# Kernel tuning notes

Measured on AMD Instinct MI355X. Metric: run time of the kernel, lower is better.

The kernel has to match this reference:

```python
import jax, jax.numpy as jnp
import numpy as np

NUM_USERS = 100000
NUM_BOOKS = 50000
HIDDEN = 128
USER_FEAT = 256
BOOK_FEAT = 256
E_PER_REL = 500000
NUM_LAYERS = 2


def setup_inputs() -> dict:
    key = jax.random.key(0)
    ks = jax.random.split(key, 10)
    user_x = jax.random.normal(ks[0], (NUM_USERS, USER_FEAT), dtype=jnp.float32)
    book_x = jax.random.normal(ks[1], (NUM_BOOKS, BOOK_FEAT), dtype=jnp.float32)
    user_W = jax.random.normal(ks[2], (HIDDEN, USER_FEAT), dtype=jnp.float32) * 0.05
    user_b = jax.random.normal(ks[3], (HIDDEN,), dtype=jnp.float32) * 0.05
    book_W = jax.random.normal(ks[4], (HIDDEN, BOOK_FEAT), dtype=jnp.float32) * 0.05
    book_b = jax.random.normal(ks[5], (HIDDEN,), dtype=jnp.float32) * 0.05
    # edge_index[0] = user indices, edge_index[1] = book indices
    rates_edge = jnp.stack([
        jax.random.randint(ks[6], (E_PER_REL,), 0, NUM_USERS),
        jax.random.randint(ks[7], (E_PER_REL,), 0, NUM_BOOKS)])
    implicit_edge = jnp.stack([
        jax.random.randint(ks[8], (E_PER_REL,), 0, NUM_USERS),
        jax.random.randint(ks[9], (E_PER_REL,), 0, NUM_BOOKS)])
    return {"user_x": user_x, "book_x": book_x, "user_W": user_W,
            "user_b": user_b, "book_W": book_W, "book_b": book_b,
            "rates_edge": rates_edge, "implicit_edge": implicit_edge}


def _lightgcn(user_x, book_x, user_W, user_b, book_W, book_b, rates_edge, implicit_edge):
    num_users = user_x.shape[0]
    num_nodes = num_users + book_x.shape[0]
    # input projections
    cu = user_x @ user_W.T + user_b  # [U, H]
    cb = book_x @ book_W.T + book_b  # [B, H]
    user_embeds = [cu]
    book_embeds = [cb]
    # build full directed edge list exactly as in the torch source
    all_edges = jnp.concatenate([rates_edge, implicit_edge], axis=1)  # [2, E]
    book_to_user = jnp.stack([all_edges[1] + num_users, all_edges[0]])
    full_edge = jnp.concatenate([all_edges, book_to_user], axis=1)  # [2, 2E]
    row, col = full_edge[0], full_edge[1]
    # symmetric degree normalization (edges fixed across layers)
    deg = jax.ops.segment_sum(jnp.ones(col.shape, dtype=cu.dtype), col,
                              num_segments=num_nodes)
    deg_inv_sqrt = jnp.where(deg > 0, jax.lax.rsqrt(jnp.maximum(deg, 1.0) * 0 + jnp.where(deg > 0, deg, 1.0)), 0.0)
    deg_inv_sqrt = jnp.where(deg > 0, jax.lax.rsqrt(jnp.where(deg > 0, deg, 1.0)), 0.0)
    norm = deg_inv_sqrt[row] * deg_inv_sqrt[col]  # [2E]
    for _ in range(NUM_LAYERS):
        x = jnp.concatenate([cu, cb], axis=0)  # [U+B, H]
        msg = x[row] * norm[:, None]           # gather + scale, [2E, H]
        out = jax.ops.segment_sum(msg, col, num_segments=num_nodes)  # scatter-add
        cu = out[:num_users]
        cb = out[num_users:]
        user_embeds.append(cu)
        book_embeds.append(cb)
    final_user = jnp.mean(jnp.stack(user_embeds), axis=0)
    final_book = jnp.mean(jnp.stack(book_embeds), axis=0)
    return final_user, final_book


def reference(user_x, book_x, user_W, user_b, book_W, book_b, rates_edge, implicit_edge):
    return _lightgcn(user_x, book_x, user_W, user_b, book_W, book_b,
                     rates_edge, implicit_edge)
```

## Files before the change

kernel.cpp:

```cpp
#include <hip/hip_runtime.h>

#define NUSERS 100000
#define NBOOKS 50000
#define HID 128
#define FEAT 256
#define EPR 500000
#define NEDGE (2 * EPR)

#define UBLK64 ((NUSERS + 63) / 64)
#define BBLK64 ((NBOOKS + 63) / 64)
#define GH_BLOCKS (UBLK64 + BBLK64)
#define FILL_B ((NEDGE + 255) / 256)
#define NXCD 8

typedef __attribute__((ext_vector_type(8))) short bf16x8;
typedef __attribute__((ext_vector_type(4))) float f32x4;

__device__ __forceinline__ unsigned short f2bf(float f) {
  union { float f; unsigned u; } v; v.f = f;
  unsigned r = v.u + 0x7FFFu + ((v.u >> 16) & 1u);
  return (unsigned short)(r >> 16);
}
__device__ __forceinline__ float bf2f(unsigned short h) {
  union { unsigned u; float f; } v; v.u = ((unsigned)h) << 16;
  return v.f;
}
__device__ __forceinline__ unsigned pk2bf(float lo, float hi) {
  unsigned r;
  asm("v_cvt_pk_bf16_f32 %0, %1, %2" : "=v"(r) : "v"(lo), "v"(hi));
  return r;
}
__device__ __forceinline__ int xcc_id() {
  unsigned id;
  asm volatile("s_getreg_b32 %0, hwreg(HW_REG_XCC_ID)" : "=s"(id));
  return (int)(id & 7);
}

__global__ void cast_w(const float* __restrict__ w0, const float* __restrict__ w1,
                       unsigned short* __restrict__ o0, unsigned short* __restrict__ o1)
{
  int i = blockIdx.x * 256 + threadIdx.x;
  if (i < HID * FEAT) { o0[i] = f2bf(w0[i]); o1[i] = f2bf(w1[i]); }
}

__device__ __forceinline__ void decode_edge(const int* __restrict__ rates,
                                            const int* __restrict__ impl,
                                            int i, int& u, int& bk)
{
  if (i < EPR) { u = rates[i]; bk = rates[EPR + i]; }
  else { int j = i - EPR; u = impl[j]; bk = impl[EPR + j]; }
}

__global__ __launch_bounds__(256) void gemm_hist(
    const float* __restrict__ Xu, const float* __restrict__ Xb,
    const unsigned short* __restrict__ Wu, const unsigned short* __restrict__ Wb,
    const float* __restrict__ bu, const float* __restrict__ bb,
    unsigned short* __restrict__ cu0b, float* __restrict__ outb,
    float* __restrict__ outu,
    const int* __restrict__ rates, const int* __restrict__ impl,
    int* __restrict__ degu8, int* __restrict__ cntb8,
    unsigned* __restrict__ relpos)
{
  __shared__ float Asb[4][2048];
  const int bid = blockIdx.x;
  const int tid = threadIdx.x;
  const int lane = tid & 63;
  const int wv   = tid >> 6;
  const int l15  = lane & 15, l4 = lane >> 4;

  {
    const unsigned x = (unsigned)xcc_id();
    int* cnt = cntb8 + (size_t)x * NBOOKS;
    int* deg = degu8 + (size_t)x * NUSERS;
    const int e0 = bid * 512 + tid;
#pragma unroll
    for (int q = 0; q < 2; ++q) {
      int e = e0 + q * 256;
      if (e < NEDGE) {
        int u, bk;
        decode_edge(rates, impl, e, u, bk);
        unsigned p = (unsigned)__hip_atomic_fetch_add(&cnt[bk], 1, __ATOMIC_RELAXED,
                                                      __HIP_MEMORY_SCOPE_WORKGROUP);
        __hip_atomic_fetch_add(&deg[u], 1, __ATOMIC_RELAXED,
                               __HIP_MEMORY_SCOPE_WORKGROUP);
        relpos[e] = (x << 29) | (p & 0x1FFFFFFFu);
      }
    }
  }

  const bool isU = bid < UBLK64;
  const float* __restrict__ X = isU ? Xu : Xb;
  const unsigned short* __restrict__ W = isU ? Wu : Wb;
  const float* __restrict__ bias = isU ? bu : bb;
  const int M    = isU ? NUSERS : NBOOKS;
  const int bm   = (isU ? bid : bid - UBLK64) * 64;
  const int wrow = bm + wv * 16;

  float* wbase = &Asb[wv][0];

  f32x4 acc[8];
#pragma unroll
  for (int ni = 0; ni < 8; ++ni) acc[ni] = (f32x4)0.f;

#pragma unroll
  for (int h = 0; h < 2; ++h) {
    if (h) {
      asm volatile("s_waitcnt lgkmcnt(0)" ::: "memory");
      __builtin_amdgcn_sched_barrier(0);
    }
#pragma unroll
    for (int rnd = 0; rnd < 8; ++rnd) {
      int o = rnd * 64 + lane;
      int r = o >> 5;
      int c = o & 31;
      int lc = c ^ r;
      int gr = wrow + r; if (gr > M - 1) gr = M - 1;
      __builtin_amdgcn_global_load_lds(
          (const float*)&X[(size_t)gr * FEAT + h * 128 + lc * 4],
          wbase + rnd * 256, 16, 0, 0);
    }
    asm volatile("s_waitcnt vmcnt(0)" ::: "memory");
    __builtin_amdgcn_sched_barrier(0);

#pragma unroll
    for (int ks = 0; ks < 4; ++ks) {
      const int kg = h * 4 + ks;
      bf16x8 bfr[8];
#pragma unroll
      for (int ni = 0; ni < 8; ++ni)
        bfr[ni] = *reinterpret_cast<const bf16x8*>(
            &W[(size_t)(ni * 16 + l15) * FEAT + kg * 32 + l4 * 8]);

      int u0 = (ks * 8 + l4 * 2) ^ l15;
      int u1 = (ks * 8 + l4 * 2 + 1) ^ l15;
      f32x4 a0 = *reinterpret_cast<const f32x4*>(&wbase[(l15 * 32 + u0) * 4]);
      f32x4 a1 = *reinterpret_cast<const f32x4*>(&wbase[(l15 * 32 + u1) * 4]);
      union { unsigned u32[4]; bf16x8 v; } au;
      au.u32[0] = pk2bf(a0[0], a0[1]);
      au.u32[1] = pk2bf(a0[2], a0[3]);
      au.u32[2] = pk2bf(a1[0], a1[1]);
      au.u32[3] = pk2bf(a1[2], a1[3]);

#pragma unroll
      for (int ni = 0; ni < 8; ++ni)
        acc[ni] = __builtin_amdgcn_mfma_f32_16x16x32_bf16(au.v, bfr[ni], acc[ni], 0, 0, 0);
    }
  }

#pragma unroll
  for (int ni = 0; ni < 8; ++ni) {
    int col = ni * 16 + l15;
    float bj = bias[col];
#pragma unroll
    for (int j = 0; j < 4; ++j) {
      int rr = wrow + l4 * 4 + j;
      if (rr < M) {
        float vv = acc[ni][j] + bj;
        if (isU) {
          cu0b[(size_t)rr * HID + col] = f2bf(vv);
          if (rr >= NBOOKS) outu[(size_t)rr * HID + col] = vv * (1.0f / 3.0f);
        } else {
          outb[(size_t)rr * HID + col] = vv * (1.0f / 3.0f);
        }
      }
    }
  }
}

__global__ void merge_dis(int* __restrict__ cntb8, const int* __restrict__ degu8,
                          int* __restrict__ cntb, float* __restrict__ dis)
{
  int i = blockIdx.x * 256 + threadIdx.x;
  if (i >= NUSERS) return;
  int d = 0;
#pragma unroll
  for (int x = 0; x < NXCD; ++x) d += degu8[(size_t)x * NUSERS + i];
  if (i < NBOOKS) {
    int run = 0;
#pragma unroll
    for (int x = 0; x < NXCD; ++x) {
      int c = cntb8[(size_t)x * NBOOKS + i];
      cntb8[(size_t)x * NBOOKS + i] = run;
      run += c;
    }
    cntb[i] = run;
    d += run;
  }
  dis[i] = (d > 0) ? rsqrtf((float)d) : 0.f;
}

__global__ void fill_scatter(const int* __restrict__ rates, const int* __restrict__ impl,
                             const int* __restrict__ offs,
                             const unsigned* __restrict__ relpos,
                             const int* __restrict__ cntb8,
                             int* __restrict__ brow)
{
  int i = blockIdx.x * 256 + threadIdx.x;
  if (i >= NEDGE) return;
  int u, bk;
  decode_edge(rates, impl, i, u, bk);
  unsigned rp = relpos[i];
  unsigned x  = (rp >> 29) & 7u;
  int rel     = (int)(rp & 0x1FFFFFFFu);
  brow[offs[bk] + cntb8[(size_t)x * NBOOKS + bk] + rel] = u;
}

__global__ __launch_bounds__(1024) void scan_blocks(const int* __restrict__ counts,
                                                    int* __restrict__ offs,
                                                    int* __restrict__ bsum, int N)
{
  __shared__ int buf[1024];
  int t = threadIdx.x;
  int i = blockIdx.x * 1024 + t;
  int v = (i < N) ? counts[i] : 0;
  buf[t] = v;
  __syncthreads();
  for (int off = 1; off < 1024; off <<= 1) {
    int x = (t >= off) ? buf[t - off] : 0;
    __syncthreads();
    buf[t] += x;
    __syncthreads();
  }
  int incl = buf[t];
  if (i < N) offs[i] = incl - v;
  if (t == 1023) bsum[blockIdx.x] = incl;
}

__global__ void scan_totals(const int* __restrict__ bsum, int* __restrict__ bpre,
                            int* __restrict__ offs, int nb, int N)
{
  if (threadIdx.x == 0 && blockIdx.x == 0) {
    int run = 0;
    for (int b = 0; b < nb; ++b) { bpre[b] = run; run += bsum[b]; }
    offs[N] = run;
  }
}

__global__ void add_prefix(int* __restrict__ offs, const int* __restrict__ bpre, int N)
{
  int i = blockIdx.x * blockDim.x + threadIdx.x;
  if (i < N) offs[i] += bpre[i >> 10];
}

__global__ __launch_bounds__(256) void pull1(const unsigned short* __restrict__ srcb,
    const int* __restrict__ offs, const int* __restrict__ brow,
    const float* __restrict__ dis, unsigned short* __restrict__ dstb)
{
  int c = (blockIdx.x << 2) + (threadIdx.x >> 6);
  if (c >= NBOOKS) return;
  const int lane = threadIdx.x & 63;
  const int g = lane >> 4, l = lane & 15;
  const int s = offs[c], e = offs[c + 1];

  float acc[8];
#pragma unroll
  for (int j = 0; j < 8; ++j) acc[j] = 0.f;

  int i = s + g;
  for (; i + 4 < e; i += 8) {
    int rr0 = brow[i], rr1 = brow[i + 4];
    float w0 = dis[rr0], w1 = dis[rr1];
    bf16x8 v0 = *reinterpret_cast<const bf16x8*>(&srcb[(size_t)rr0 * HID + l * 8]);
    bf16x8 v1 = *reinterpret_cast<const bf16x8*>(&srcb[(size_t)rr1 * HID + l * 8]);
#pragma unroll
    for (int j = 0; j < 8; ++j) acc[j] += w0 * bf2f((unsigned short)v0[j]);
#pragma unroll
    for (int j = 0; j < 8; ++j) acc[j] += w1 * bf2f((unsigned short)v1[j]);
  }
  if (i < e) {
    int rr = brow[i];
    float w = dis[rr];
    bf16x8 v = *reinterpret_cast<const bf16x8*>(&srcb[(size_t)rr * HID + l * 8]);
#pragma unroll
    for (int j = 0; j < 8; ++j) acc[j] += w * bf2f((unsigned short)v[j]);
  }

#pragma unroll
  for (int j = 0; j < 8; ++j) {
    acc[j] += __shfl_xor(acc[j], 16, 64);
    acc[j] += __shfl_xor(acc[j], 32, 64);
  }
  if (g == 0) {
    float db = dis[c];
    bf16x8 o;
#pragma unroll
    for (int j = 0; j < 8; ++j) o[j] = (short)f2bf(db * acc[j]);
    *reinterpret_cast<bf16x8*>(&dstb[(size_t)c * HID + l * 8]) = o;
  }
}

__global__ __launch_bounds__(256) void pull2_final(const unsigned short* __restrict__ h1b,
    const int* __restrict__ offs, const int* __restrict__ brow,
    const float* __restrict__ dis, const unsigned short* __restrict__ cu0b,
    float* __restrict__ outu)
{
  int c = (blockIdx.x << 2) + (threadIdx.x >> 6);
  if (c >= NBOOKS) return;
  const int lane = threadIdx.x & 63;
  const int g = lane >> 4, l = lane & 15;
  const int s = offs[c], e = offs[c + 1];

  float acc[8];
#pragma unroll
  for (int j = 0; j < 8; ++j) acc[j] = 0.f;

  int i = s + g;
  for (; i + 4 < e; i += 8) {
    int rr0 = brow[i], rr1 = brow[i + 4];
    int rc0 = rr0 < NBOOKS ? rr0 : 0;
    int rc1 = rr1 < NBOOKS ? rr1 : 0;
    float w0 = rr0 < NBOOKS ? dis[rr0] : 0.f;
    float w1 = rr1 < NBOOKS ? dis[rr1] : 0.f;
    bf16x8 v0 = *reinterpret_cast<const bf16x8*>(&h1b[(size_t)rc0 * HID + l * 8]);
    bf16x8 v1 = *reinterpret_cast<const bf16x8*>(&h1b[(size_t)rc1 * HID + l * 8]);
#pragma unroll
    for (int j = 0; j < 8; ++j) acc[j] += w0 * bf2f((unsigned short)v0[j]);
#pragma unroll
    for (int j = 0; j < 8; ++j) acc[j] += w1 * bf2f((unsigned short)v1[j]);
  }
  if (i < e) {
    int rr = brow[i];
    int rc = rr < NBOOKS ? rr : 0;
    float w = rr < NBOOKS ? dis[rr] : 0.f;
    bf16x8 v = *reinterpret_cast<const bf16x8*>(&h1b[(size_t)rc * HID + l * 8]);
#pragma unroll
    for (int j = 0; j < 8; ++j) acc[j] += w * bf2f((unsigned short)v[j]);
  }

#pragma unroll
  for (int j = 0; j < 8; ++j) {
    acc[j] += __shfl_xor(acc[j], 16, 64);
    acc[j] += __shfl_xor(acc[j], 32, 64);
  }
  if (g == 0) {
    float db = dis[c];
    size_t idx = (size_t)c * HID + l * 8;
    bf16x8 c0 = *reinterpret_cast<const bf16x8*>(&cu0b[idx]);
    bf16x8 h1 = *reinterpret_cast<const bf16x8*>(&h1b[idx]);
    float r[8];
#pragma unroll
    for (int j = 0; j < 8; ++j)
      r[j] = (bf2f((unsigned short)c0[j]) + bf2f((unsigned short)h1[j]) + db * acc[j]) * (1.0f / 3.0f);
    *reinterpret_cast<float4*>(&outu[idx])     = make_float4(r[0], r[1], r[2], r[3]);
    *reinterpret_cast<float4*>(&outu[idx + 4]) = make_float4(r[4], r[5], r[6], r[7]);
  }
}

extern "C" void kernel_launch(void* const* d_in, const int* in_sizes, int n_in,
                              void* d_out, int out_size, void* d_ws, size_t ws_size,
                              hipStream_t stream)
{
  const float* user_x = (const float*)d_in[0];
  const float* book_x = (const float*)d_in[1];
  const float* user_W = (const float*)d_in[2];
  const float* user_b = (const float*)d_in[3];
  const float* book_W = (const float*)d_in[4];
  const float* book_b = (const float*)d_in[5];
  const int*   rates  = (const int*)d_in[6];
  const int*   impl   = (const int*)d_in[7];

  float* out      = (float*)d_out;
  float* out_user = out;
  float* out_book = out + (size_t)NUSERS * HID;

  char* p = (char*)d_ws;
  auto carve = [&](size_t bytes) -> void* {
    void* r = (void*)p;
    p += (bytes + 255) & ~(size_t)255;
    return r;
  };
  unsigned short* cu0b   = (unsigned short*)carve((size_t)NUSERS * HID * 2);
  unsigned short* h1b    = (unsigned short*)carve((size_t)NBOOKS * HID * 2);
  unsigned short* wub    = (unsigned short*)carve((size_t)HID * FEAT * 2);
  unsigned short* wbb    = (unsigned short*)carve((size_t)HID * FEAT * 2);
  int*      degu8  = (int*)carve((size_t)NXCD * NUSERS * 4);
  int*      cntb8  = (int*)carve((size_t)NXCD * NBOOKS * 4);
  int*      cntb   = (int*)carve((size_t)NBOOKS * 4);
  float*    dis    = (float*)carve((size_t)NUSERS * 4);
  int*      offs   = (int*)carve((size_t)(NBOOKS + 2) * 4);
  int*      bsum   = (int*)carve(256 * 4);
  int*      bpre   = (int*)carve(256 * 4);
  unsigned* relpos = (unsigned*)carve((size_t)NEDGE * 4);
  int*      brow   = (int*)carve((size_t)NEDGE * 4);

  hipMemsetAsync(degu8, 0, (size_t)NXCD * NUSERS * 4, stream);
  hipMemsetAsync(cntb8, 0, (size_t)NXCD * NBOOKS * 4, stream);

  cast_w<<<(HID * FEAT + 255) / 256, 256, 0, stream>>>(user_W, book_W, wub, wbb);

  gemm_hist<<<GH_BLOCKS, 256, 0, stream>>>(
      user_x, book_x, wub, wbb, user_b, book_b,
      cu0b, out_book, out_user, rates, impl, degu8, cntb8, relpos);

  merge_dis<<<(NUSERS + 255) / 256, 256, 0, stream>>>(cntb8, degu8, cntb, dis);

  const int nb = (NBOOKS + 1023) / 1024;
  scan_blocks<<<nb, 1024, 0, stream>>>(cntb, offs, bsum, NBOOKS);
  scan_totals<<<1, 64, 0, stream>>>(bsum, bpre, offs, nb, NBOOKS);
  add_prefix<<<(NBOOKS + 255) / 256, 256, 0, stream>>>(offs, bpre, NBOOKS);

  fill_scatter<<<FILL_B, 256, 0, stream>>>(rates, impl, offs, relpos, cntb8, brow);

  pull1<<<(NBOOKS + 3) / 4, 256, 0, stream>>>(cu0b, offs, brow, dis, h1b);
  pull2_final<<<(NBOOKS + 3) / 4, 256, 0, stream>>>(h1b, offs, brow, dis, cu0b, out_user);
}
```

Before: 288.3 us.

## Replace per-XCD global atomic histograms with chunked LDS histograms

Edge degree counting and per-book rank assignment move out of the GEMM kernel into a separate hist64 kernel. That kernel uses 64 chunks of 16K edges, each running LDS atomic histograms over several passes of 16K-bin segments. The aim is to remove contended global atomics and the two memsets, while keeping stable per-chunk ranks for the CSR fill. In exchange there is an extra serial kernel with only 64 blocks and 11 passes over the edges each. The merge also reads much larger per-chunk count arrays.

New measurement: 296.3 us. 1.03x slower.

```diff
diff --git a/kernel.cpp b/kernel.cpp
--- a/kernel.cpp
+++ b/kernel.cpp
@@ -9,9 +9,16 @@
 
 #define UBLK64 ((NUSERS + 63) / 64)
 #define BBLK64 ((NBOOKS + 63) / 64)
-#define GH_BLOCKS (UBLK64 + BBLK64)
+#define GEMM_BLOCKS (UBLK64 + BBLK64)
 #define FILL_B ((NEDGE + 255) / 256)
-#define NXCD 8
+
+#define NCHUNK 64
+#define CHUNK 16384
+#define BINS 16384
+#define BOOK_SP 4
+#define USER_SP 7
+#define HB_STRIDE (BOOK_SP * BINS)
+#define HU_STRIDE (USER_SP * BINS)
 
 typedef __attribute__((ext_vector_type(8))) short bf16x8;
 typedef __attribute__((ext_vector_type(4))) float f32x4;
@@ -30,11 +37,6 @@
   asm("v_cvt_pk_bf16_f32 %0, %1, %2" : "=v"(r) : "v"(lo), "v"(hi));
   return r;
 }
-__device__ __forceinline__ int xcc_id() {
-  unsigned id;
-  asm volatile("s_getreg_b32 %0, hwreg(HW_REG_XCC_ID)" : "=s"(id));
-  return (int)(id & 7);
-}
 
 __global__ void cast_w(const float* __restrict__ w0, const float* __restrict__ w1,
                        unsigned short* __restrict__ o0, unsigned short* __restrict__ o1)
@@ -51,15 +53,12 @@
   else { int j = i - EPR; u = impl[j]; bk = impl[EPR + j]; }
 }
 
-__global__ __launch_bounds__(256) void gemm_hist(
+__global__ __launch_bounds__(256) void gemm_all(
     const float* __restrict__ Xu, const float* __restrict__ Xb,
     const unsigned short* __restrict__ Wu, const unsigned short* __restrict__ Wb,
     const float* __restrict__ bu, const float* __restrict__ bb,
     unsigned short* __restrict__ cu0b, float* __restrict__ outb,
-    float* __restrict__ outu,
-    const int* __restrict__ rates, const int* __restrict__ impl,
-    int* __restrict__ degu8, int* __restrict__ cntb8,
-    unsigned* __restrict__ relpos)
+    float* __restrict__ outu)
 {
   __shared__ float Asb[4][2048];
   const int bid = blockIdx.x;
@@ -67,26 +66,6 @@
   const int lane = tid & 63;
   const int wv   = tid >> 6;
   const int l15  = lane & 15, l4 = lane >> 4;
-
-  {
-    const unsigned x = (unsigned)xcc_id();
-    int* cnt = cntb8 + (size_t)x * NBOOKS;
-    int* deg = degu8 + (size_t)x * NUSERS;
-    const int e0 = bid * 512 + tid;
-#pragma unroll
-    for (int q = 0; q < 2; ++q) {
-      int e = e0 + q * 256;
-      if (e < NEDGE) {
-        int u, bk;
-        decode_edge(rates, impl, e, u, bk);
-        unsigned p = (unsigned)__hip_atomic_fetch_add(&cnt[bk], 1, __ATOMIC_RELAXED,
-                                                      __HIP_MEMORY_SCOPE_WORKGROUP);
-        __hip_atomic_fetch_add(&deg[u], 1, __ATOMIC_RELAXED,
-                               __HIP_MEMORY_SCOPE_WORKGROUP);
-        relpos[e] = (x << 29) | (p & 0x1FFFFFFFu);
-      }
-    }
-  }
 
   const bool isU = bid < UBLK64;
   const float* __restrict__ X = isU ? Xu : Xb;
@@ -167,23 +146,68 @@
   }
 }
 
-__global__ void merge_dis(int* __restrict__ cntb8, const int* __restrict__ degu8,
+__global__ __launch_bounds__(1024) void hist64(
+    const int* __restrict__ rates, const int* __restrict__ impl,
+    unsigned* __restrict__ hb, unsigned* __restrict__ hu,
+    unsigned short* __restrict__ rank16)
+{
+  __shared__ unsigned h[BINS];
+  const int c = blockIdx.x;
+  const int t = threadIdx.x;
+  const int e0 = c * CHUNK;
+  int eN = NEDGE - e0;
+  if (eN > CHUNK) eN = CHUNK;
+  if (eN < 0) eN = 0;
+
+  for (int p = 0; p < BOOK_SP; ++p) {
+    for (int j = t; j < BINS; j += 1024) h[j] = 0;
+    __syncthreads();
+    for (int k = t; k < eN; k += 1024) {
+      int e = e0 + k;
+      int bk = (e < EPR) ? rates[EPR + e] : impl[EPR + (e - EPR)];
+      if ((bk >> 14) == p) {
+        unsigned r = atomicAdd(&h[bk & (BINS - 1)], 1u);
+        rank16[e] = (unsigned short)r;
+      }
+    }
+    __syncthreads();
+    unsigned* dst = hb + (size_t)c * HB_STRIDE + (p << 14);
+    for (int j = t; j < BINS; j += 1024) dst[j] = h[j];
+    __syncthreads();
+  }
+
+  for (int q = 0; q < USER_SP; ++q) {
+    for (int j = t; j < BINS; j += 1024) h[j] = 0;
+    __syncthreads();
+    for (int k = t; k < eN; k += 1024) {
+      int e = e0 + k;
+      int u = (e < EPR) ? rates[e] : impl[e - EPR];
+      if ((u >> 14) == q) atomicAdd(&h[u & (BINS - 1)], 1u);
+    }
+    __syncthreads();
+    unsigned* dst = hu + (size_t)c * HU_STRIDE + (q << 14);
+    for (int j = t; j < BINS; j += 1024) dst[j] = h[j];
+    __syncthreads();
+  }
+}
+
+__global__ void merge_dis(unsigned* __restrict__ hb, const unsigned* __restrict__ hu,
                           int* __restrict__ cntb, float* __restrict__ dis)
 {
   int i = blockIdx.x * 256 + threadIdx.x;
   if (i >= NUSERS) return;
-  int d = 0;
-#pragma unroll
-  for (int x = 0; x < NXCD; ++x) d += degu8[(size_t)x * NUSERS + i];
+  unsigned d = 0;
+#pragma unroll 8
+  for (int c = 0; c < NCHUNK; ++c) d += hu[(size_t)c * HU_STRIDE + i];
   if (i < NBOOKS) {
-    int run = 0;
-#pragma unroll
-    for (int x = 0; x < NXCD; ++x) {
-      int c = cntb8[(size_t)x * NBOOKS + i];
-      cntb8[(size_t)x * NBOOKS + i] = run;
-      run += c;
-    }
-    cntb[i] = run;
+    unsigned run = 0;
+#pragma unroll 8
+    for (int c = 0; c < NCHUNK; ++c) {
+      unsigned v = hb[(size_t)c * HB_STRIDE + i];
+      hb[(size_t)c * HB_STRIDE + i] = run;
+      run += v;
+    }
+    cntb[i] = (int)run;
     d += run;
   }
   dis[i] = (d > 0) ? rsqrtf((float)d) : 0.f;
@@ -191,18 +215,16 @@
 
 __global__ void fill_scatter(const int* __restrict__ rates, const int* __restrict__ impl,
                              const int* __restrict__ offs,
-                             const unsigned* __restrict__ relpos,
-                             const int* __restrict__ cntb8,
+                             const unsigned* __restrict__ hb,
+                             const unsigned short* __restrict__ rank16,
                              int* __restrict__ brow)
 {
-  int i = blockIdx.x * 256 + threadIdx.x;
-  if (i >= NEDGE) return;
+  int e = blockIdx.x * 256 + threadIdx.x;
+  if (e >= NEDGE) return;
   int u, bk;
-  decode_edge(rates, impl, i, u, bk);
-  unsigned rp = relpos[i];
-  unsigned x  = (rp >> 29) & 7u;
-  int rel     = (int)(rp & 0x1FFFFFFFu);
-  brow[offs[bk] + cntb8[(size_t)x * NBOOKS + bk] + rel] = u;
+  decode_edge(rates, impl, e, u, bk);
+  int c = e >> 14;
+  brow[offs[bk] + (int)hb[(size_t)c * HB_STRIDE + bk] + (int)rank16[e]] = u;
 }
 
 __global__ __launch_bounds__(1024) void scan_blocks(const int* __restrict__ counts,
@@ -373,33 +395,31 @@
   unsigned short* h1b    = (unsigned short*)carve((size_t)NBOOKS * HID * 2);
   unsigned short* wub    = (unsigned short*)carve((size_t)HID * FEAT * 2);
   unsigned short* wbb    = (unsigned short*)carve((size_t)HID * FEAT * 2);
-  int*      degu8  = (int*)carve((size_t)NXCD * NUSERS * 4);
-  int*      cntb8  = (int*)carve((size_t)NXCD * NBOOKS * 4);
-  int*      cntb   = (int*)carve((size_t)NBOOKS * 4);
-  float*    dis    = (float*)carve((size_t)NUSERS * 4);
-  int*      offs   = (int*)carve((size_t)(NBOOKS + 2) * 4);
-  int*      bsum   = (int*)carve(256 * 4);
-  int*      bpre   = (int*)carve(256 * 4);
-  unsigned* relpos = (unsigned*)carve((size_t)NEDGE * 4);
-  int*      brow   = (int*)carve((size_t)NEDGE * 4);
-
-  hipMemsetAsync(degu8, 0, (size_t)NXCD * NUSERS * 4, stream);
-  hipMemsetAsync(cntb8, 0, (size_t)NXCD * NBOOKS * 4, stream);
+  unsigned*       hb     = (unsigned*)carve((size_t)NCHUNK * HB_STRIDE * 4);
+  unsigned*       hu     = (unsigned*)carve((size_t)NCHUNK * HU_STRIDE * 4);
+  unsigned short* rank16 = (unsigned short*)carve((size_t)NEDGE * 2);
+  int*            cntb   = (int*)carve((size_t)NBOOKS * 4);
+  float*          dis    = (float*)carve((size_t)NUSERS * 4);
+  int*            offs   = (int*)carve((size_t)(NBOOKS + 2) * 4);
+  int*            bsum   = (int*)carve(256 * 4);
+  int*            bpre   = (int*)carve(256 * 4);
+  int*            brow   = (int*)carve((size_t)NEDGE * 4);
 
   cast_w<<<(HID * FEAT + 255) / 256, 256, 0, stream>>>(user_W, book_W, wub, wbb);
 
-  gemm_hist<<<GH_BLOCKS, 256, 0, stream>>>(
-      user_x, book_x, wub, wbb, user_b, book_b,
-      cu0b, out_book, out_user, rates, impl, degu8, cntb8, relpos);
-
-  merge_dis<<<(NUSERS + 255) / 256, 256, 0, stream>>>(cntb8, degu8, cntb, dis);
+  gemm_all<<<GEMM_BLOCKS, 256, 0, stream>>>(
+      user_x, book_x, wub, wbb, user_b, book_b, cu0b, out_book, out_user);
+
+  hist64<<<NCHUNK, 1024, 0, stream>>>(rates, impl, hb, hu, rank16);
+
+  merge_dis<<<(NUSERS + 255) / 256, 256, 0, stream>>>(hb, hu, cntb, dis);
 
   const int nb = (NBOOKS + 1023) / 1024;
   scan_blocks<<<nb, 1024, 0, stream>>>(cntb, offs, bsum, NBOOKS);
   scan_totals<<<1, 64, 0, stream>>>(bsum, bpre, offs, nb, NBOOKS);
   add_prefix<<<(NBOOKS + 255) / 256, 256, 0, stream>>>(offs, bpre, NBOOKS);
 
-  fill_scatter<<<FILL_B, 256, 0, stream>>>(rates, impl, offs, relpos, cntb8, brow);
+  fill_scatter<<<FILL_B, 256, 0, stream>>>(rates, impl, offs, hb, rank16, brow);
 
   pull1<<<(NBOOKS + 3) / 4, 256, 0, stream>>>(cu0b, offs, brow, dis, h1b);
   pull2_final<<<(NBOOKS + 3) / 4, 256, 0, stream>>>(h1b, offs, brow, dis, cu0b, out_user);
```
